# Kernel optimization log

Measured on AMD Instinct MI355X. Metric: run time of the kernel, lower is better.

The kernel has to match this reference:

```python
import jax, jax.numpy as jnp
import numpy as np

N_NODES = 50000
N_EDGES = 1000000
D_IN = 128
HID = 64
N_GRAPHS = 256
NEG_SLOPE = 0.2


def _gatv2_layer(x, src, dst, Wl, Wr, att, b, n_nodes):
    # lin_l applied to source nodes, lin_r to target nodes (PyG GATv2Conv, heads=1)
    xl = x @ Wl.T  # [N, C]
    xr = x @ Wr.T  # [N, C]
    e = jax.nn.leaky_relu(xl[src] + xr[dst], NEG_SLOPE)  # [E, C]
    logits = e @ att  # [E]
    # segment softmax over destination node
    m = jax.ops.segment_max(logits, dst, num_segments=n_nodes)
    ex = jnp.exp(logits - m[dst])
    den = jax.ops.segment_sum(ex, dst, num_segments=n_nodes)
    alpha = ex / den[dst]  # [E]
    out = jax.ops.segment_sum(alpha[:, None] * xl[src], dst, num_segments=n_nodes)
    return out + b


def setup_inputs() -> dict:
    key = jax.random.key(0)
    ks = jax.random.split(key, 32)
    x = jax.random.normal(ks[0], (N_NODES, D_IN), dtype=jnp.float32)
    edge_index = jax.random.randint(ks[1], (2, N_EDGES), 0, N_NODES, dtype=jnp.int64)
    batch = jnp.sort(jax.random.randint(ks[2], (N_NODES,), 0, N_GRAPHS, dtype=jnp.int64))
    inp = {"x": x, "edge_index": edge_index, "batch": batch}
    dims = [D_IN, HID, HID]  # input dim per layer
    kidx = 3
    for i, din in enumerate(dims):
        inp[f"Wl{i}"] = jax.random.normal(ks[kidx], (HID, din), dtype=jnp.float32) * 0.1; kidx += 1
        inp[f"Wr{i}"] = jax.random.normal(ks[kidx], (HID, din), dtype=jnp.float32) * 0.1; kidx += 1
        inp[f"att{i}"] = jax.random.normal(ks[kidx], (HID,), dtype=jnp.float32) * 0.1; kidx += 1
        inp[f"b{i}"] = jnp.zeros((HID,), dtype=jnp.float32)
        inp[f"Rw{i}"] = jax.random.normal(ks[kidx], (HID, din), dtype=jnp.float32) * 0.1; kidx += 1
        inp[f"Rb{i}"] = jnp.zeros((HID,), dtype=jnp.float32)
    inp["Wf"] = jax.random.normal(ks[kidx], (1, HID), dtype=jnp.float32) * 0.1
    inp["bf"] = jnp.zeros((1,), dtype=jnp.float32)
    return inp


def reference(x, edge_index, batch, Wl0, Wr0, att0, b0, Rw0, Rb0,
              Wl1, Wr1, att1, b1, Rw1, Rb1,
              Wl2, Wr2, att2, b2, Rw2, Rb2, Wf, bf):
    n = x.shape[0]
    # add_self_loops=True (PyG default)
    loops = jnp.arange(n, dtype=edge_index.dtype)
    src = jnp.concatenate([edge_index[0], loops])
    dst = jnp.concatenate([edge_index[1], loops])
    layers = [(Wl0, Wr0, att0, b0, Rw0, Rb0),
              (Wl1, Wr1, att1, b1, Rw1, Rb1),
              (Wl2, Wr2, att2, b2, Rw2, Rb2)]
    for i, (Wl, Wr, att, b, Rw, Rb) in enumerate(layers):
        h = _gatv2_layer(x, src, dst, Wl, Wr, att, b, n) + (x @ Rw.T + Rb)  # res=True
        # norm=None -> Identity; dropout inactive at inference
        x = jax.nn.relu(h) if i < len(layers) - 1 else h
    # global_mean_pool
    sums = jax.ops.segment_sum(x, batch, num_segments=N_GRAPHS)
    cnt = jax.ops.segment_sum(jnp.ones((n,), x.dtype), batch, num_segments=N_GRAPHS)
    pooled = sums / jnp.maximum(cnt, 1.0)[:, None]
    return pooled @ Wf.T + bf
```

## Files before the change

kernel.cpp:

```cpp
#include <hip/hip_runtime.h>


#define NN 50000
#define NE 1000000
#define HID 64
#define DIN0 128
#define NG 256
#define NEG 0.2f

#define SCHUNK 1024
#define SNB ((NN + SCHUNK - 1) / SCHUNK)

typedef float f32x4 __attribute__((ext_vector_type(4)));
typedef short s8v __attribute__((ext_vector_type(8)));
typedef short s4v __attribute__((ext_vector_type(4)));
typedef __bf16 bf16x8 __attribute__((ext_vector_type(8)));
typedef _Float16 h2v __attribute__((ext_vector_type(2)));
typedef unsigned u32x2 __attribute__((ext_vector_type(2)));
typedef unsigned short u16;

__device__ __forceinline__ unsigned short f2bf(float f) {
    unsigned u = __float_as_uint(f);
    u = u + 0x7fffu + ((u >> 16) & 1u);
    return (unsigned short)(u >> 16);
}
__device__ __forceinline__ float bf2f(unsigned short v) {
    return __uint_as_float(((unsigned)v) << 16);
}
__device__ __forceinline__ short split_hi(float x) {
    return (short)f2bf(x);
}
__device__ __forceinline__ short split_lo(float x, short hi) {
    return (short)f2bf(x - bf2f((unsigned short)hi));
}
__device__ __forceinline__ h2v u2h(unsigned u) { return __builtin_bit_cast(h2v, u); }
__device__ __forceinline__ unsigned h2u(h2v h) { return __builtin_bit_cast(unsigned, h); }
__device__ __forceinline__ h2v pklo(unsigned a, unsigned b) {
    return u2h(__builtin_amdgcn_perm(b, a, 0x05040100u));
}
__device__ __forceinline__ h2v pkhi(unsigned a, unsigned b) {
    return u2h(__builtin_amdgcn_perm(b, a, 0x07060302u));
}
__device__ __forceinline__ float red32_add(float v) {
    unsigned u = __float_as_uint(v);
    u32x2 r = __builtin_amdgcn_permlane32_swap(u, u, false, false);
    return __uint_as_float(r[0]) + __uint_as_float(r[1]);
}
__device__ __forceinline__ float red32_max(float v) {
    unsigned u = __float_as_uint(v);
    u32x2 r = __builtin_amdgcn_permlane32_swap(u, u, false, false);
    return fmaxf(__uint_as_float(r[0]), __uint_as_float(r[1]));
}

__global__ __launch_bounds__(256) void k_wt_all(
        const float* __restrict__ Wl0, const float* __restrict__ Wr0, const float* __restrict__ Rw0,
        const float* __restrict__ Wl1, const float* __restrict__ Wr1, const float* __restrict__ Rw1,
        const float* __restrict__ Wl2, const float* __restrict__ Wr2, const float* __restrict__ Rw2,
        const float* __restrict__ att0, const float* __restrict__ att1, const float* __restrict__ att2,
        short* __restrict__ Ws0, short* __restrict__ Ws1, short* __restrict__ Ws2,
        _Float16* __restrict__ attp,
        int* __restrict__ startg, int* __restrict__ endg) {
    int i = blockIdx.x * 256 + threadIdx.x;
    if (i < 2 * NG) {
        if (i < NG) startg[i] = 0; else endg[i - NG] = 0;
    }
    if (i < 3 * HID) {
        int L = i >> 6, c = i & 63;
        const float* at = (L == 0) ? att0 : (L == 1) ? att1 : att2;
        float a = at[c];
        attp[L * 2 * HID + c] = (_Float16)(0.6f * a);
        attp[L * 2 * HID + HID + c] = (_Float16)(0.4f * a);
    }
    const int L0N = 3 * HID * DIN0;
    const int L1N = 3 * HID * HID;
    if (i >= L0N + 2 * L1N) return;
    const float* Wm; short* Ws; int din, local;
    if (i < L0N) {
        local = i; din = DIN0; Ws = Ws0;
        int m = local / (DIN0 * HID);
        Wm = (m == 0) ? Wl0 : (m == 1) ? Wr0 : Rw0;
    } else if (i < L0N + L1N) {
        local = i - L0N; din = HID; Ws = Ws1;
        int m = local / (HID * HID);
        Wm = (m == 0) ? Wl1 : (m == 1) ? Wr1 : Rw1;
    } else {
        local = i - L0N - L1N; din = HID; Ws = Ws2;
        int m = local / (HID * HID);
        Wm = (m == 0) ? Wl2 : (m == 1) ? Wr2 : Rw2;
    }
    int m = local / (din * HID);
    int r = local - m * (din * HID);
    int c = r / din, k = r - c * din;
    float w = Wm[c * din + k];
    short hi = split_hi(w);
    short lo = split_lo(w, hi);
    Ws[(((m * 2 + 0) * HID + c) * din) + k] = hi;
    Ws[(((m * 2 + 1) * HID + c) * din) + k] = lo;
}

__global__ void k_bounds(const int* __restrict__ batch,
                         int* __restrict__ startg, int* __restrict__ endg,
                         int* __restrict__ cnt8) {
    int i = blockIdx.x * 256 + threadIdx.x;
    if (i >= NN) return;
#pragma unroll
    for (int g = 0; g < 8; g++) cnt8[g * NN + i] = 0;
    int g = batch[i];
    if (i == 0 || batch[i - 1] != g) startg[g] = i;
    if (i == NN - 1 || batch[i + 1] != g) endg[g] = i + 1;
}

__global__ __launch_bounds__(256) void k_hist8(const int* __restrict__ edst,
                                               int* __restrict__ cnt8,
                                               u16* __restrict__ rank) {
    int* mycnt = cnt8 + (blockIdx.x & 7) * NN;
    for (int e = blockIdx.x * 256 + threadIdx.x; e < NE; e += 512 * 256) {
        int r = atomicAdd(&mycnt[edst[e]], 1);
        rank[e] = (u16)r;
    }
}

__global__ void k_hist_red(int* __restrict__ cnt8, int* __restrict__ cnt) {
    int i = blockIdx.x * 256 + threadIdx.x;
    if (i >= NN) return;
    int s = 1;
#pragma unroll
    for (int g = 0; g < 8; g++) {
        int t = cnt8[g * NN + i];
        cnt8[g * NN + i] = s;
        s += t;
    }
    cnt[i] = s;
}

__global__ __launch_bounds__(256) void k_scan_part(const int* __restrict__ cnt,
                                                   int* __restrict__ part) {
    __shared__ int ws[4];
    int b = blockIdx.x, t = threadIdx.x;
    int i0 = b * SCHUNK + t * 4;
    int s = 0;
#pragma unroll
    for (int j = 0; j < 4; j++) {
        int i = i0 + j;
        if (i < NN) s += cnt[i];
    }
#pragma unroll
    for (int o = 32; o; o >>= 1) s += __shfl_xor(s, o, 64);
    if ((t & 63) == 0) ws[t >> 6] = s;
    __syncthreads();
    if (t == 0) part[b] = ws[0] + ws[1] + ws[2] + ws[3];
}

__global__ void k_scan_small(const int* __restrict__ part, int* __restrict__ partScan) {
    __shared__ int sh[SNB];
    int t = threadIdx.x;
    if (t < SNB) sh[t] = part[t];
    __syncthreads();
    if (t < SNB) {
        int s = 0;
        for (int i = 0; i < t; i++) s += sh[i];
        partScan[t] = s;
    }
}

__global__ __launch_bounds__(256) void k_scan_emit(const int* __restrict__ cnt,
                                                   const int* __restrict__ partScan,
                                                   int* __restrict__ off,
                                                   u16* __restrict__ srcs) {
    __shared__ int tsum[256];
    int b = blockIdx.x, t = threadIdx.x;
    int i0 = b * SCHUNK + t * 4;
    int e[4], p[4];
    int s = 0;
#pragma unroll
    for (int j = 0; j < 4; j++) {
        int i = i0 + j;
        e[j] = (i < NN) ? cnt[i] : 0;
        p[j] = s;
        s += e[j];
    }
    tsum[t] = s;
    __syncthreads();
    for (int d = 1; d < 256; d <<= 1) {
        int v = (t >= d) ? tsum[t - d] : 0;
        __syncthreads();
        tsum[t] += v;
        __syncthreads();
    }
    int base = partScan[b] + ((t == 0) ? 0 : tsum[t - 1]);
#pragma unroll
    for (int j = 0; j < 4; j++) {
        int i = i0 + j;
        if (i < NN) {
            int v = base + p[j];
            off[i] = v;
            srcs[v] = (u16)i;
            if (i == NN - 1) off[NN] = v + e[j];
        }
    }
}

__global__ __launch_bounds__(256) void k_scatter_rank(
        const int* __restrict__ esrc, const int* __restrict__ edst,
        const int* __restrict__ off, const int* __restrict__ cnt8,
        const u16* __restrict__ rank, u16* __restrict__ srcs) {
    int e = blockIdx.x * 256 + threadIdx.x;
    if (e >= NE) return;
    int d = edst[e];
    int slice = (e >> 8) & 7;
    int pos = off[d] + cnt8[slice * NN + d] + (int)rank[e];
    srcs[pos] = (u16)esrc[e];
}

template <int DIN, bool RELU>
__global__ __launch_bounds__(256, 3) void k_gemm(
        const float* __restrict__ xin, const short* __restrict__ Ws,
        const float* __restrict__ bvec, const float* __restrict__ rb,
        _Float16* __restrict__ xl16, _Float16* __restrict__ xr16, float* __restrict__ acc) {
    constexpr int LROW = 40;
    __shared__ short lds[20480];
    short* xhi = lds;
    short* xlo = lds + 2560;

    const int tid = threadIdx.x;
    const int w = tid >> 6;
    const int lane = tid & 63;
    const int col = lane & 15;
    const int quad = lane >> 4;
    const int nb0 = blockIdx.x * 64;

    f32x4 d[3][4];
#pragma unroll
    for (int m = 0; m < 3; m++)
#pragma unroll
        for (int ct = 0; ct < 4; ct++) d[m][ct] = (f32x4){0.f, 0.f, 0.f, 0.f};

    for (int c0 = 0; c0 < DIN; c0 += 32) {
        if (c0) __syncthreads();
        for (int u = tid; u < 512; u += 256) {
            int row = u >> 3, kq = u & 7;
            int n = nb0 + row;
            float4 v = make_float4(0.f, 0.f, 0.f, 0.f);
            if (n < NN) {
                v = *(const float4*)&xin[(size_t)n * DIN + c0 + 4 * kq];
                if (RELU) {
                    v.x = fmaxf(v.x, 0.f); v.y = fmaxf(v.y, 0.f);
                    v.z = fmaxf(v.z, 0.f); v.w = fmaxf(v.w, 0.f);
                }
            }
            s4v h, l;
            short h0 = split_hi(v.x), l0 = split_lo(v.x, h0);
            short h1 = split_hi(v.y), l1 = split_lo(v.y, h1);
            short h2 = split_hi(v.z), l2 = split_lo(v.z, h2);
            short h3 = split_hi(v.w), l3 = split_lo(v.w, h3);
            h[0] = h0; h[1] = h1; h[2] = h2; h[3] = h3;
            l[0] = l0; l[1] = l1; l[2] = l2; l[3] = l3;
            *(s4v*)&xhi[row * LROW + 4 * kq] = h;
            *(s4v*)&xlo[row * LROW + 4 * kq] = l;
        }
        for (int u = tid; u < 1536; u += 256) {
            int mp = u >> 8;
            int r = u & 255;
            int c = r >> 2, q = r & 3;
            s8v v = *(const s8v*)&Ws[((mp * HID + c) * DIN) + c0 + 8 * q];
            *(s8v*)&lds[5120 + mp * 2560 + c * LROW + 8 * q] = v;
        }
        __syncthreads();

        bf16x8 a_h = __builtin_bit_cast(bf16x8,
            *(const s8v*)&xhi[(w * 16 + col) * LROW + quad * 8]);
        bf16x8 a_l = __builtin_bit_cast(bf16x8,
            *(const s8v*)&xlo[(w * 16 + col) * LROW + quad * 8]);

#pragma unroll
        for (int m = 0; m < 3; m++) {
#pragma unroll
            for (int ct = 0; ct < 4; ct++) {
                bf16x8 b_h = __builtin_bit_cast(bf16x8,
                    *(const s8v*)&lds[5120 + (m * 2 + 0) * 2560 + (ct * 16 + col) * LROW + quad * 8]);
                bf16x8 b_l = __builtin_bit_cast(bf16x8,
                    *(const s8v*)&lds[5120 + (m * 2 + 1) * 2560 + (ct * 16 + col) * LROW + quad * 8]);
                d[m][ct] = __builtin_amdgcn_mfma_f32_16x16x32_bf16(a_h, b_h, d[m][ct], 0, 0, 0);
                d[m][ct] = __builtin_amdgcn_mfma_f32_16x16x32_bf16(a_h, b_l, d[m][ct], 0, 0, 0);
                d[m][ct] = __builtin_amdgcn_mfma_f32_16x16x32_bf16(a_l, b_h, d[m][ct], 0, 0, 0);
            }
        }
    }

#pragma unroll
    for (int r = 0; r < 4; r++) {
        int n = nb0 + w * 16 + quad * 4 + r;
        if (n >= NN) continue;
        size_t base = (size_t)n * HID;
#pragma unroll
        for (int ct = 0; ct < 4; ct++) {
            int c = ct * 16 + col;
            xl16[base + c] = (_Float16)d[0][ct][r];
            xr16[base + c] = (_Float16)d[1][ct][r];
            acc[base + c] = d[2][ct][r] + bvec[c] + rb[c];
        }
    }
}

__global__ __launch_bounds__(256) void k_attn_dst(
        const int* __restrict__ off, const u16* __restrict__ srcs,
        const _Float16* __restrict__ xl16, const _Float16* __restrict__ xr16,
        const _Float16* __restrict__ attL, float* __restrict__ acc) {
    const int lane = threadIdx.x & 63;
    const int d = blockIdx.x * 4 + (threadIdx.x >> 6);
    if (d >= NN) return;
    const int e = lane >> 3;
    const int cg = lane & 7;

    const int lo = off[d], deg = off[d + 1] - lo;

    uint4 X = *(const uint4*)&xr16[(size_t)d * HID + 8 * cg];
    uint4 A6 = *(const uint4*)&attL[8 * cg];
    uint4 A4 = *(const uint4*)&attL[HID + 8 * cg];
    h2v xh0 = u2h(X.x), xh1 = u2h(X.y), xh2 = u2h(X.z), xh3 = u2h(X.w);
    h2v a60 = u2h(A6.x), a61 = u2h(A6.y), a62 = u2h(A6.z), a63 = u2h(A6.w);
    h2v a40 = u2h(A4.x), a41 = u2h(A4.y), a42 = u2h(A4.z), a43 = u2h(A4.w);

#define EDGE_LOGIT(S, U, T)                                                    \
    {                                                                          \
        U = *(const uint4*)&xl16[(size_t)(S) * HID + 8 * cg];                  \
        h2v _v; unsigned _a; float _ps;                                        \
        _v = u2h(U.x) + xh0; _a = h2u(_v) & 0x7FFF7FFFu;                       \
        _ps = __builtin_amdgcn_fdot2(a60, _v, 0.f, false);                     \
        _ps = __builtin_amdgcn_fdot2(a40, u2h(_a), _ps, false);                \
        _v = u2h(U.y) + xh1; _a = h2u(_v) & 0x7FFF7FFFu;                       \
        _ps = __builtin_amdgcn_fdot2(a61, _v, _ps, false);                     \
        _ps = __builtin_amdgcn_fdot2(a41, u2h(_a), _ps, false);                \
        _v = u2h(U.z) + xh2; _a = h2u(_v) & 0x7FFF7FFFu;                       \
        _ps = __builtin_amdgcn_fdot2(a62, _v, _ps, false);                     \
        _ps = __builtin_amdgcn_fdot2(a42, u2h(_a), _ps, false);                \
        _v = u2h(U.w) + xh3; _a = h2u(_v) & 0x7FFF7FFFu;                       \
        _ps = __builtin_amdgcn_fdot2(a63, _v, _ps, false);                     \
        _ps = __builtin_amdgcn_fdot2(a43, u2h(_a), _ps, false);                \
        _ps += __shfl_xor(_ps, 1, 64);                                         \
        _ps += __shfl_xor(_ps, 2, 64);                                         \
        _ps += __shfl_xor(_ps, 4, 64);                                         \
        T = _ps;                                                               \
    }

    float m = -INFINITY, l = 0.f;
    float4 oA = make_float4(0.f, 0.f, 0.f, 0.f);
    float4 oB = make_float4(0.f, 0.f, 0.f, 0.f);

    for (int base = 0; base < deg; base += 32) {
        const int rem = deg - base;
        int s0 = (int)srcs[lo + min(base + e, deg - 1)];
        int s1 = (int)srcs[lo + min(base + 8 + e, deg - 1)];

        uint4 U0, U1, U2, U3;
        float t0, t1, t2 = -INFINITY, t3 = -INFINITY;
        EDGE_LOGIT(s0, U0, t0);
        EDGE_LOGIT(s1, U1, t1);
        if (base + e >= deg) t0 = -INFINITY;
        if (base + 8 + e >= deg) t1 = -INFINITY;

        const bool do2 = rem > 16;
        if (do2) {
            int s2 = (int)srcs[lo + min(base + 16 + e, deg - 1)];
            EDGE_LOGIT(s2, U2, t2);
            if (base + 16 + e >= deg) t2 = -INFINITY;
            if (rem > 24) {
                int s3 = (int)srcs[lo + min(base + 24 + e, deg - 1)];
                EDGE_LOGIT(s3, U3, t3);
                if (base + 24 + e >= deg) t3 = -INFINITY;
            } else {
                U3 = U0;
            }
        }

        float cm = fmaxf(fmaxf(t0, t1), fmaxf(t2, t3));
        cm = fmaxf(cm, __shfl_xor(cm, 8, 64));
        cm = fmaxf(cm, __shfl_xor(cm, 16, 64));
        cm = red32_max(cm);
        if (cm > m) {
            float corr = __expf(m - cm);
            m = cm;
            l *= corr;
            oA.x *= corr; oA.y *= corr; oA.z *= corr; oA.w *= corr;
            oB.x *= corr; oB.y *= corr; oB.z *= corr; oB.w *= corr;
        }
        float p0 = __expf(t0 - m);
        float p1 = __expf(t1 - m);
        l += p0 + p1;
        h2v p01 = {(_Float16)p0, (_Float16)p1};
        oA.x = __builtin_amdgcn_fdot2(p01, pklo(U0.x, U1.x), oA.x, false);
        oA.y = __builtin_amdgcn_fdot2(p01, pkhi(U0.x, U1.x), oA.y, false);
        oA.z = __builtin_amdgcn_fdot2(p01, pklo(U0.y, U1.y), oA.z, false);
        oA.w = __builtin_amdgcn_fdot2(p01, pkhi(U0.y, U1.y), oA.w, false);
        oB.x = __builtin_amdgcn_fdot2(p01, pklo(U0.z, U1.z), oB.x, false);
        oB.y = __builtin_amdgcn_fdot2(p01, pkhi(U0.z, U1.z), oB.y, false);
        oB.z = __builtin_amdgcn_fdot2(p01, pklo(U0.w, U1.w), oB.z, false);
        oB.w = __builtin_amdgcn_fdot2(p01, pkhi(U0.w, U1.w), oB.w, false);
        if (do2) {
            float p2 = __expf(t2 - m);
            float p3 = __expf(t3 - m);
            l += p2 + p3;
            h2v p23 = {(_Float16)p2, (_Float16)p3};
            oA.x = __builtin_amdgcn_fdot2(p23, pklo(U2.x, U3.x), oA.x, false);
            oA.y = __builtin_amdgcn_fdot2(p23, pkhi(U2.x, U3.x), oA.y, false);
            oA.z = __builtin_amdgcn_fdot2(p23, pklo(U2.y, U3.y), oA.z, false);
            oA.w = __builtin_amdgcn_fdot2(p23, pkhi(U2.y, U3.y), oA.w, false);
            oB.x = __builtin_amdgcn_fdot2(p23, pklo(U2.z, U3.z), oB.x, false);
            oB.y = __builtin_amdgcn_fdot2(p23, pkhi(U2.z, U3.z), oB.y, false);
            oB.z = __builtin_amdgcn_fdot2(p23, pklo(U2.w, U3.w), oB.z, false);
            oB.w = __builtin_amdgcn_fdot2(p23, pkhi(U2.w, U3.w), oB.w, false);
        }
    }
#undef EDGE_LOGIT

#pragma unroll
    for (int w = 8; w <= 16; w <<= 1) {
        l    += __shfl_xor(l, w, 64);
        oA.x += __shfl_xor(oA.x, w, 64); oA.y += __shfl_xor(oA.y, w, 64);
        oA.z += __shfl_xor(oA.z, w, 64); oA.w += __shfl_xor(oA.w, w, 64);
        oB.x += __shfl_xor(oB.x, w, 64); oB.y += __shfl_xor(oB.y, w, 64);
        oB.z += __shfl_xor(oB.z, w, 64); oB.w += __shfl_xor(oB.w, w, 64);
    }
    l    = red32_add(l);
    oA.x = red32_add(oA.x); oA.y = red32_add(oA.y);
    oA.z = red32_add(oA.z); oA.w = red32_add(oA.w);
    oB.x = red32_add(oB.x); oB.y = red32_add(oB.y);
    oB.z = red32_add(oB.z); oB.w = red32_add(oB.w);

    if (e == 0) {
        float inv = 1.f / l;
        float4* a4 = (float4*)&acc[(size_t)d * HID + 8 * cg];
        float4 c0 = a4[0], c1 = a4[1];
        c0.x += oA.x * inv; c0.y += oA.y * inv;
        c0.z += oA.z * inv; c0.w += oA.w * inv;
        c1.x += oB.x * inv; c1.y += oB.y * inv;
        c1.z += oB.z * inv; c1.w += oB.w * inv;
        a4[0] = c0; a4[1] = c1;
    }
}

__global__ __launch_bounds__(512) void k_pool_final(
        const float* __restrict__ acc,
        const int* __restrict__ startg, const int* __restrict__ endg,
        const float* __restrict__ Wf, const float* __restrict__ bf_,
        float* __restrict__ out) {
    __shared__ float red[8][HID];
    const int g = blockIdx.x;
    const int c = threadIdx.x & 63;
    const int j = threadIdx.x >> 6;
    const int s = startg[g], epos = endg[g];

    float sum = 0.f;
    for (int n = s + j; n < epos; n += 8)
        sum += acc[(size_t)n * HID + c];
    red[j][c] = sum;
    __syncthreads();

    if (threadIdx.x < HID) {
        float tot = 0.f;
#pragma unroll
        for (int w = 0; w < 8; w++) tot += red[w][c];
        float cntf = (float)(epos - s);
        float v = tot / fmaxf(cntf, 1.f) * Wf[c];
#pragma unroll
        for (int o = 32; o; o >>= 1) v += __shfl_xor(v, o, 64);
        if (c == 0) out[g] = v + bf_[0];
    }
}

extern "C" void kernel_launch(void* const* d_in, const int* in_sizes, int n_in,
                              void* d_out, int out_size, void* d_ws, size_t ws_size,
                              hipStream_t stream) {
    const float* x   = (const float*)d_in[0];
    const int* eidx  = (const int*)d_in[1];
    const int* batch = (const int*)d_in[2];
    const int* esrc = eidx;
    const int* edst = eidx + NE;
    const float* Wf  = (const float*)d_in[21];
    const float* bfb = (const float*)d_in[22];

    float* wsf = (float*)d_ws;
    const size_t NN64 = (size_t)NN * HID;
    _Float16* xl16 = (_Float16*)wsf;
    _Float16* xr16 = (_Float16*)(wsf + NN64);
    float* acc0   = wsf + 2 * NN64;
    float* acc1   = acc0 + NN64;
    short* Ws0    = (short*)(acc1 + NN64);
    short* Ws1    = Ws0 + 2 * 3 * HID * DIN0;
    short* Ws2    = Ws1 + 2 * 3 * HID * HID;
    int*   ccnt   = (int*)(Ws2 + 2 * 3 * HID * HID);
    int*   startg = ccnt + NN;
    int*   endg   = startg + NG;
    int*   off    = endg + NG;
    int*   part   = off + NN + 1;
    int*   partSc = part + SNB;
    int*   cnt8   = partSc + SNB;
    u16*   rank   = (u16*)(cnt8 + 8 * NN);
    u16*   srcs   = rank + NE;
    _Float16* attp = (_Float16*)(srcs + NE + NN);

    k_wt_all<<<(3 * HID * DIN0 + 2 * 3 * HID * HID + 255) / 256, 256, 0, stream>>>(
        (const float*)d_in[3], (const float*)d_in[4], (const float*)d_in[7],
        (const float*)d_in[9], (const float*)d_in[10], (const float*)d_in[13],
        (const float*)d_in[15], (const float*)d_in[16], (const float*)d_in[19],
        (const float*)d_in[5], (const float*)d_in[11], (const float*)d_in[17],
        Ws0, Ws1, Ws2, attp, startg, endg);
    k_bounds<<<(NN + 255) / 256, 256, 0, stream>>>(batch, startg, endg, cnt8);

    k_hist8<<<512, 256, 0, stream>>>(edst, cnt8, rank);
    k_hist_red<<<(NN + 255) / 256, 256, 0, stream>>>(cnt8, ccnt);
    k_scan_part<<<SNB, 256, 0, stream>>>(ccnt, part);
    k_scan_small<<<1, 64, 0, stream>>>(part, partSc);
    k_scan_emit<<<SNB, 256, 0, stream>>>(ccnt, partSc, off, srcs);
    k_scatter_rank<<<(NE + 255) / 256, 256, 0, stream>>>(esrc, edst, off, cnt8, rank, srcs);

    const short* Wss[3] = {Ws0, Ws1, Ws2};
    float* accs[4] = {acc0, acc0, acc1, acc0};
    const int gemm_grid = (NN + 63) / 64;
    for (int L = 0; L < 3; L++) {
        const float* b   = (const float*)d_in[3 + L * 6 + 3];
        const float* Rb  = (const float*)d_in[3 + L * 6 + 5];
        float* accOut = accs[L + 1];

        if (L == 0)
            k_gemm<DIN0, false><<<gemm_grid, 256, 0, stream>>>(
                x, Wss[0], b, Rb, xl16, xr16, accOut);
        else
            k_gemm<HID, true><<<gemm_grid, 256, 0, stream>>>(
                accs[L], Wss[L], b, Rb, xl16, xr16, accOut);

        k_attn_dst<<<(NN + 3) / 4, 256, 0, stream>>>(
            off, srcs, xl16, xr16, attp + L * 2 * HID, accOut);
    }

    k_pool_final<<<NG, 512, 0, stream>>>(accs[3], startg, endg, Wf, bfb, (float*)d_out);
}
```

Before: 347.3 us.

## Make attention kernel persistent with prefetch of next node's offsets and sources

The per-destination attention kernel becomes a grid-stride persistent kernel with 2048 blocks. Each wave prefetches the next node's CSR offsets, xr row and first 32 source indices while it processes the current node, so index-load latency overlaps with compute. A fast path for nodes with degree at most 32 skips the online-softmax rescaling loop. The cost is higher register pressure and possibly lower occupancy, and with a fixed grid some waves may get more work than others.

```diff
diff --git a/kernel.cpp b/kernel.cpp
--- a/kernel.cpp
+++ b/kernel.cpp
@@ -10,6 +10,9 @@
 
 #define SCHUNK 1024
 #define SNB ((NN + SCHUNK - 1) / SCHUNK)
+
+#define ATTN_BLK 2048
+#define ATTN_WAVES (ATTN_BLK * 4)
 
 typedef float f32x4 __attribute__((ext_vector_type(4)));
 typedef short s8v __attribute__((ext_vector_type(8)));
@@ -307,17 +310,12 @@
         const _Float16* __restrict__ xl16, const _Float16* __restrict__ xr16,
         const _Float16* __restrict__ attL, float* __restrict__ acc) {
     const int lane = threadIdx.x & 63;
-    const int d = blockIdx.x * 4 + (threadIdx.x >> 6);
-    if (d >= NN) return;
     const int e = lane >> 3;
     const int cg = lane & 7;
-
-    const int lo = off[d], deg = off[d + 1] - lo;
-
-    uint4 X = *(const uint4*)&xr16[(size_t)d * HID + 8 * cg];
+    const int W = blockIdx.x * 4 + (threadIdx.x >> 6);
+
     uint4 A6 = *(const uint4*)&attL[8 * cg];
     uint4 A4 = *(const uint4*)&attL[HID + 8 * cg];
-    h2v xh0 = u2h(X.x), xh1 = u2h(X.y), xh2 = u2h(X.z), xh3 = u2h(X.w);
     h2v a60 = u2h(A6.x), a61 = u2h(A6.y), a62 = u2h(A6.z), a63 = u2h(A6.w);
     h2v a40 = u2h(A4.x), a41 = u2h(A4.y), a42 = u2h(A4.z), a43 = u2h(A4.w);
 
@@ -343,100 +341,187 @@
         T = _ps;                                                               \
     }
 
-    float m = -INFINITY, l = 0.f;
-    float4 oA = make_float4(0.f, 0.f, 0.f, 0.f);
-    float4 oB = make_float4(0.f, 0.f, 0.f, 0.f);
-
-    for (int base = 0; base < deg; base += 32) {
-        const int rem = deg - base;
-        int s0 = (int)srcs[lo + min(base + e, deg - 1)];
-        int s1 = (int)srcs[lo + min(base + 8 + e, deg - 1)];
-
-        uint4 U0, U1, U2, U3;
-        float t0, t1, t2 = -INFINITY, t3 = -INFINITY;
-        EDGE_LOGIT(s0, U0, t0);
-        EDGE_LOGIT(s1, U1, t1);
-        if (base + e >= deg) t0 = -INFINITY;
-        if (base + 8 + e >= deg) t1 = -INFINITY;
-
-        const bool do2 = rem > 16;
-        if (do2) {
-            int s2 = (int)srcs[lo + min(base + 16 + e, deg - 1)];
-            EDGE_LOGIT(s2, U2, t2);
-            if (base + 16 + e >= deg) t2 = -INFINITY;
-            if (rem > 24) {
-                int s3 = (int)srcs[lo + min(base + 24 + e, deg - 1)];
-                EDGE_LOGIT(s3, U3, t3);
-                if (base + 24 + e >= deg) t3 = -INFINITY;
-            } else {
-                U3 = U0;
+    int d = W;
+    int lo = off[d];
+    int deg = off[d + 1] - lo;
+    uint4 X = *(const uint4*)&xr16[(size_t)d * HID + 8 * cg];
+    int s0p = (int)srcs[lo + min(e, deg - 1)];
+    int s1p = (int)srcs[lo + min(8 + e, deg - 1)];
+    int s2p = (int)srcs[lo + min(16 + e, deg - 1)];
+    int s3p = (int)srcs[lo + min(24 + e, deg - 1)];
+
+    while (true) {
+        const int dn = d + ATTN_WAVES;
+        int lo_n = 0, deg_n = 1;
+        uint4 Xn = X;
+        if (dn < NN) {
+            lo_n = off[dn];
+            deg_n = off[dn + 1] - lo_n;
+            Xn = *(const uint4*)&xr16[(size_t)dn * HID + 8 * cg];
+        }
+
+        h2v xh0 = u2h(X.x), xh1 = u2h(X.y), xh2 = u2h(X.z), xh3 = u2h(X.w);
+
+        float l;
+        float4 oA, oB;
+
+        if (deg <= 32) {
+            uint4 U0, U1, U2, U3;
+            float t0, t1, t2 = -INFINITY, t3 = -INFINITY;
+            EDGE_LOGIT(s0p, U0, t0);
+            EDGE_LOGIT(s1p, U1, t1);
+            if (e >= deg) t0 = -INFINITY;
+            if (8 + e >= deg) t1 = -INFINITY;
+            const bool do2 = deg > 16;
+            if (do2) {
+                EDGE_LOGIT(s2p, U2, t2);
+                if (16 + e >= deg) t2 = -INFINITY;
+                if (deg > 24) {
+                    EDGE_LOGIT(s3p, U3, t3);
+                    if (24 + e >= deg) t3 = -INFINITY;
+                } else {
+                    U3 = U0;
+                }
             }
-        }
-
-        float cm = fmaxf(fmaxf(t0, t1), fmaxf(t2, t3));
-        cm = fmaxf(cm, __shfl_xor(cm, 8, 64));
-        cm = fmaxf(cm, __shfl_xor(cm, 16, 64));
-        cm = red32_max(cm);
-        if (cm > m) {
-            float corr = __expf(m - cm);
-            m = cm;
-            l *= corr;
-            oA.x *= corr; oA.y *= corr; oA.z *= corr; oA.w *= corr;
-            oB.x *= corr; oB.y *= corr; oB.z *= corr; oB.w *= corr;
-        }
-        float p0 = __expf(t0 - m);
-        float p1 = __expf(t1 - m);
-        l += p0 + p1;
-        h2v p01 = {(_Float16)p0, (_Float16)p1};
-        oA.x = __builtin_amdgcn_fdot2(p01, pklo(U0.x, U1.x), oA.x, false);
-        oA.y = __builtin_amdgcn_fdot2(p01, pkhi(U0.x, U1.x), oA.y, false);
-        oA.z = __builtin_amdgcn_fdot2(p01, pklo(U0.y, U1.y), oA.z, false);
-        oA.w = __builtin_amdgcn_fdot2(p01, pkhi(U0.y, U1.y), oA.w, false);
-        oB.x = __builtin_amdgcn_fdot2(p01, pklo(U0.z, U1.z), oB.x, false);
-        oB.y = __builtin_amdgcn_fdot2(p01, pkhi(U0.z, U1.z), oB.y, false);
-        oB.z = __builtin_amdgcn_fdot2(p01, pklo(U0.w, U1.w), oB.z, false);
-        oB.w = __builtin_amdgcn_fdot2(p01, pkhi(U0.w, U1.w), oB.w, false);
-        if (do2) {
-            float p2 = __expf(t2 - m);
-            float p3 = __expf(t3 - m);
-            l += p2 + p3;
-            h2v p23 = {(_Float16)p2, (_Float16)p3};
-            oA.x = __builtin_amdgcn_fdot2(p23, pklo(U2.x, U3.x), oA.x, false);
-            oA.y = __builtin_amdgcn_fdot2(p23, pkhi(U2.x, U3.x), oA.y, false);
-            oA.z = __builtin_amdgcn_fdot2(p23, pklo(U2.y, U3.y), oA.z, false);
-            oA.w = __builtin_amdgcn_fdot2(p23, pkhi(U2.y, U3.y), oA.w, false);
-            oB.x = __builtin_amdgcn_fdot2(p23, pklo(U2.z, U3.z), oB.x, false);
-            oB.y = __builtin_amdgcn_fdot2(p23, pkhi(U2.z, U3.z), oB.y, false);
-            oB.z = __builtin_amdgcn_fdot2(p23, pklo(U2.w, U3.w), oB.z, false);
-            oB.w = __builtin_amdgcn_fdot2(p23, pkhi(U2.w, U3.w), oB.w, false);
-        }
+            float cm = fmaxf(fmaxf(t0, t1), fmaxf(t2, t3));
+            cm = fmaxf(cm, __shfl_xor(cm, 8, 64));
+            cm = fmaxf(cm, __shfl_xor(cm, 16, 64));
+            cm = red32_max(cm);
+            float p0 = __expf(t0 - cm);
+            float p1 = __expf(t1 - cm);
+            l = p0 + p1;
+            h2v p01 = {(_Float16)p0, (_Float16)p1};
+            oA.x = __builtin_amdgcn_fdot2(p01, pklo(U0.x, U1.x), 0.f, false);
+            oA.y = __builtin_amdgcn_fdot2(p01, pkhi(U0.x, U1.x), 0.f, false);
+            oA.z = __builtin_amdgcn_fdot2(p01, pklo(U0.y, U1.y), 0.f, false);
+            oA.w = __builtin_amdgcn_fdot2(p01, pkhi(U0.y, U1.y), 0.f, false);
+            oB.x = __builtin_amdgcn_fdot2(p01, pklo(U0.z, U1.z), 0.f, false);
+            oB.y = __builtin_amdgcn_fdot2(p01, pkhi(U0.z, U1.z), 0.f, false);
+            oB.z = __builtin_amdgcn_fdot2(p01, pklo(U0.w, U1.w), 0.f, false);
+            oB.w = __builtin_amdgcn_fdot2(p01, pkhi(U0.w, U1.w), 0.f, false);
+            if (do2) {
+                float p2 = __expf(t2 - cm);
+                float p3 = __expf(t3 - cm);
+                l += p2 + p3;
+                h2v p23 = {(_Float16)p2, (_Float16)p3};
+                oA.x = __builtin_amdgcn_fdot2(p23, pklo(U2.x, U3.x), oA.x, false);
+                oA.y = __builtin_amdgcn_fdot2(p23, pkhi(U2.x, U3.x), oA.y, false);
+                oA.z = __builtin_amdgcn_fdot2(p23, pklo(U2.y, U3.y), oA.z, false);
+                oA.w = __builtin_amdgcn_fdot2(p23, pkhi(U2.y, U3.y), oA.w, false);
+                oB.x = __builtin_amdgcn_fdot2(p23, pklo(U2.z, U3.z), oB.x, false);
+                oB.y = __builtin_amdgcn_fdot2(p23, pkhi(U2.z, U3.z), oB.y, false);
+                oB.z = __builtin_amdgcn_fdot2(p23, pklo(U2.w, U3.w), oB.z, false);
+                oB.w = __builtin_amdgcn_fdot2(p23, pkhi(U2.w, U3.w), oB.w, false);
+            }
+        } else {
+            float m = -INFINITY;
+            l = 0.f;
+            oA = make_float4(0.f, 0.f, 0.f, 0.f);
+            oB = make_float4(0.f, 0.f, 0.f, 0.f);
+            for (int base = 0; base < deg; base += 32) {
+                const int rem = deg - base;
+                int s0 = (int)srcs[lo + min(base + e, deg - 1)];
+                int s1 = (int)srcs[lo + min(base + 8 + e, deg - 1)];
+
+                uint4 U0, U1, U2, U3;
+                float t0, t1, t2 = -INFINITY, t3 = -INFINITY;
+                EDGE_LOGIT(s0, U0, t0);
+                EDGE_LOGIT(s1, U1, t1);
+                if (base + e >= deg) t0 = -INFINITY;
+                if (base + 8 + e >= deg) t1 = -INFINITY;
+
+                const bool do2 = rem > 16;
+                if (do2) {
+                    int s2 = (int)srcs[lo + min(base + 16 + e, deg - 1)];
+                    EDGE_LOGIT(s2, U2, t2);
+                    if (base + 16 + e >= deg) t2 = -INFINITY;
+                    if (rem > 24) {
+                        int s3 = (int)srcs[lo + min(base + 24 + e, deg - 1)];
+                        EDGE_LOGIT(s3, U3, t3);
+                        if (base + 24 + e >= deg) t3 = -INFINITY;
+                    } else {
+                        U3 = U0;
+                    }
+                }
+
+                float cm = fmaxf(fmaxf(t0, t1), fmaxf(t2, t3));
+                cm = fmaxf(cm, __shfl_xor(cm, 8, 64));
+                cm = fmaxf(cm, __shfl_xor(cm, 16, 64));
+                cm = red32_max(cm);
+                if (cm > m) {
+                    float corr = __expf(m - cm);
+                    m = cm;
+                    l *= corr;
+                    oA.x *= corr; oA.y *= corr; oA.z *= corr; oA.w *= corr;
+                    oB.x *= corr; oB.y *= corr; oB.z *= corr; oB.w *= corr;
+                }
+                float p0 = __expf(t0 - m);
+                float p1 = __expf(t1 - m);
+                l += p0 + p1;
+                h2v p01 = {(_Float16)p0, (_Float16)p1};
+                oA.x = __builtin_amdgcn_fdot2(p01, pklo(U0.x, U1.x), oA.x, false);
+                oA.y = __builtin_amdgcn_fdot2(p01, pkhi(U0.x, U1.x), oA.y, false);
+                oA.z = __builtin_amdgcn_fdot2(p01, pklo(U0.y, U1.y), oA.z, false);
+                oA.w = __builtin_amdgcn_fdot2(p01, pkhi(U0.y, U1.y), oA.w, false);
+                oB.x = __builtin_amdgcn_fdot2(p01, pklo(U0.z, U1.z), oB.x, false);
+                oB.y = __builtin_amdgcn_fdot2(p01, pkhi(U0.z, U1.z), oB.y, false);
+                oB.z = __builtin_amdgcn_fdot2(p01, pklo(U0.w, U1.w), oB.z, false);
+                oB.w = __builtin_amdgcn_fdot2(p01, pkhi(U0.w, U1.w), oB.w, false);
+                if (do2) {
+                    float p2 = __expf(t2 - m);
+                    float p3 = __expf(t3 - m);
+                    l += p2 + p3;
+                    h2v p23 = {(_Float16)p2, (_Float16)p3};
+                    oA.x = __builtin_amdgcn_fdot2(p23, pklo(U2.x, U3.x), oA.x, false);
+                    oA.y = __builtin_amdgcn_fdot2(p23, pkhi(U2.x, U3.x), oA.y, false);
+                    oA.z = __builtin_amdgcn_fdot2(p23, pklo(U2.y, U3.y), oA.z, false);
+                    oA.w = __builtin_amdgcn_fdot2(p23, pkhi(U2.y, U3.y), oA.w, false);
+                    oB.x = __builtin_amdgcn_fdot2(p23, pklo(U2.z, U3.z), oB.x, false);
+                    oB.y = __builtin_amdgcn_fdot2(p23, pkhi(U2.z, U3.z), oB.y, false);
+                    oB.z = __builtin_amdgcn_fdot2(p23, pklo(U2.w, U3.w), oB.z, false);
+                    oB.w = __builtin_amdgcn_fdot2(p23, pkhi(U2.w, U3.w), oB.w, false);
+                }
+            }
+        }
+
+        int s0n = 0, s1n = 0, s2n = 0, s3n = 0;
+        if (dn < NN) {
+            s0n = (int)srcs[lo_n + min(e, deg_n - 1)];
+            s1n = (int)srcs[lo_n + min(8 + e, deg_n - 1)];
+            s2n = (int)srcs[lo_n + min(16 + e, deg_n - 1)];
+            s3n = (int)srcs[lo_n + min(24 + e, deg_n - 1)];
+        }
+
+#pragma unroll
+        for (int w = 8; w <= 16; w <<= 1) {
+            l    += __shfl_xor(l, w, 64);
+            oA.x += __shfl_xor(oA.x, w, 64); oA.y += __shfl_xor(oA.y, w, 64);
+            oA.z += __shfl_xor(oA.z, w, 64); oA.w += __shfl_xor(oA.w, w, 64);
+            oB.x += __shfl_xor(oB.x, w, 64); oB.y += __shfl_xor(oB.y, w, 64);
+            oB.z += __shfl_xor(oB.z, w, 64); oB.w += __shfl_xor(oB.w, w, 64);
+        }
+        l    = red32_add(l);
+        oA.x = red32_add(oA.x); oA.y = red32_add(oA.y);
+        oA.z = red32_add(oA.z); oA.w = red32_add(oA.w);
+        oB.x = red32_add(oB.x); oB.y = red32_add(oB.y);
+        oB.z = red32_add(oB.z); oB.w = red32_add(oB.w);
+
+        if (e == 0) {
+            float inv = 1.f / l;
+            float4* a4 = (float4*)&acc[(size_t)d * HID + 8 * cg];
+            float4 c0 = a4[0], c1 = a4[1];
+            c0.x += oA.x * inv; c0.y += oA.y * inv;
+            c0.z += oA.z * inv; c0.w += oA.w * inv;
+            c1.x += oB.x * inv; c1.y += oB.y * inv;
+            c1.z += oB.z * inv; c1.w += oB.w * inv;
+            a4[0] = c0; a4[1] = c1;
+        }
+
+        if (dn >= NN) break;
+        d = dn; lo = lo_n; deg = deg_n; X = Xn;
+        s0p = s0n; s1p = s1n; s2p = s2n; s3p = s3n;
     }
 #undef EDGE_LOGIT
-
-#pragma unroll
-    for (int w = 8; w <= 16; w <<= 1) {
-        l    += __shfl_xor(l, w, 64);
-        oA.x += __shfl_xor(oA.x, w, 64); oA.y += __shfl_xor(oA.y, w, 64);
-        oA.z += __shfl_xor(oA.z, w, 64); oA.w += __shfl_xor(oA.w, w, 64);
-        oB.x += __shfl_xor(oB.x, w, 64); oB.y += __shfl_xor(oB.y, w, 64);
-        oB.z += __shfl_xor(oB.z, w, 64); oB.w += __shfl_xor(oB.w, w, 64);
-    }
-    l    = red32_add(l);
-    oA.x = red32_add(oA.x); oA.y = red32_add(oA.y);
-    oA.z = red32_add(oA.z); oA.w = red32_add(oA.w);
-    oB.x = red32_add(oB.x); oB.y = red32_add(oB.y);
-    oB.z = red32_add(oB.z); oB.w = red32_add(oB.w);
-
-    if (e == 0) {
-        float inv = 1.f / l;
-        float4* a4 = (float4*)&acc[(size_t)d * HID + 8 * cg];
-        float4 c0 = a4[0], c1 = a4[1];
-        c0.x += oA.x * inv; c0.y += oA.y * inv;
-        c0.z += oA.z * inv; c0.w += oA.w * inv;
-        c1.x += oB.x * inv; c1.y += oB.y * inv;
-        c1.z += oB.z * inv; c1.w += oB.w * inv;
-        a4[0] = c0; a4[1] = c1;
-    }
 }
 
 __global__ __launch_bounds__(512) void k_pool_final(
@@ -529,7 +614,7 @@
             k_gemm<HID, true><<<gemm_grid, 256, 0, stream>>>(
                 accs[L], Wss[L], b, Rb, xl16, xr16, accOut);
 
-        k_attn_dst<<<(NN + 3) / 4, 256, 0, stream>>>(
+        k_attn_dst<<<ATTN_BLK, 256, 0, stream>>>(
             off, srcs, xl16, xr16, attp + L * 2 * HID, accOut);
     }
 
```

New measurement: 360.5 us. 1.04x slower.
